# Performance work log

Measured on AMD Instinct MI355X. Metric: run time of the kernel, lower is better.

## Reference

```python
import jax, jax.numpy as jnp
import numpy as np

B, N, F_IN, F_OUT, H = 8, 1024, 256, 256, 4
HD = F_OUT // H  # head_dim = 64
NEG_SLOPE = 0.2


def setup_inputs() -> dict:
    key = jax.random.key(0)
    k1, k2, k3 = jax.random.split(key, 3)
    x = jax.random.normal(k1, (B, N, F_IN), dtype=jnp.float32)
    adj = jnp.ones((B, N, N), dtype=jnp.int32)
    # Linear weight, stored as [in, out] so h = x @ W
    W = jax.random.normal(k2, (F_IN, F_OUT), dtype=jnp.float32) / np.sqrt(F_IN)
    # attention vector a: [H, 2*head_dim], xavier-ish init
    a = jax.random.normal(k3, (H, 2 * HD), dtype=jnp.float32) * np.sqrt(2.0 / (H + 2 * HD))
    return {"x": x, "adj": adj, "W": W, "a": a}


def reference(x, adj, W, a):
    Bq, Nq, _ = x.shape
    h = (x @ W).reshape(Bq, Nq, H, HD).transpose(0, 2, 1, 3)  # [B,H,N,HD]
    a1, a2 = a[:, :HD], a[:, HD:]  # decompose concat: e_nm = h_n.a1 + h_m.a2
    s1 = jnp.einsum('bhnd,hd->bhn', h, a1)
    s2 = jnp.einsum('bhmd,hd->bhm', h, a2)
    e = jax.nn.leaky_relu(s1[:, :, :, None] + s2[:, :, None, :], NEG_SLOPE)  # [B,H,N,N]
    e = jnp.where(adj[:, None, :, :] == 0, -jnp.inf, e)
    attention = jax.nn.softmax(e, axis=-1)
    out = jnp.einsum('bhnm,bhmd->bhnd', attention, h)
    return out.transpose(0, 2, 1, 3).reshape(Bq, Nq, H * HD)
```

## Files before the change

### kernel.cpp

```cpp
#include <hip/hip_runtime.h>
#include <math.h>

#define H 4
#define HD 64
#define NN 1024
#define BB 8
#define FIN 256
#define FOUT 256

typedef _Float16 f16x8 __attribute__((ext_vector_type(8)));
typedef _Float16 f16x4 __attribute__((ext_vector_type(4)));
typedef _Float16 f16x2 __attribute__((ext_vector_type(2)));
typedef float f32x4 __attribute__((ext_vector_type(4)));

__global__ __launch_bounds__(256) void prep(const int* __restrict__ adj,
                                            unsigned* __restrict__ adjP,
                                            const float* __restrict__ W,
                                            _Float16* __restrict__ WT) {
  __shared__ float tile[64][68];
  const int tid = threadIdx.x;
  if (blockIdx.x < 1024) {
    size_t widx = (size_t)blockIdx.x * 256 + tid;
    const int4* p = (const int4*)adj + widx * 8;
    int4 v[8];
#pragma unroll
    for (int i = 0; i < 8; ++i) v[i] = p[i];
    unsigned bits = 0;
#pragma unroll
    for (int i = 0; i < 8; ++i) {
      bits |= (v[i].x != 0 ? 1u : 0u) << (4 * i);
      bits |= (v[i].y != 0 ? 2u : 0u) << (4 * i);
      bits |= (v[i].z != 0 ? 4u : 0u) << (4 * i);
      bits |= (v[i].w != 0 ? 8u : 0u) << (4 * i);
    }
    adjP[widx] = bits;
  } else {
    const int bx = blockIdx.x - 1024;
    const int k0 = (bx & 3) * 64, f0 = (bx >> 2) * 64;
    const int r = tid >> 4, c4 = (tid & 15) * 4;
#pragma unroll
    for (int p = 0; p < 4; ++p) {
      float4 v = *(const float4*)&W[(size_t)(k0 + p * 16 + r) * FOUT + f0 + c4];
      *(float4*)&tile[p * 16 + r][c4] = v;
    }
    __syncthreads();
    const int f = tid >> 2, kg = (tid & 3) * 16;
#pragma unroll
    for (int i = 0; i < 4; ++i) {
      f16x4 o;
#pragma unroll
      for (int j = 0; j < 4; ++j) o[j] = (_Float16)tile[kg + i * 4 + j][f];
      *(f16x4*)&WT[(size_t)(f0 + f) * FIN + k0 + kg + i * 4] = o;
    }
  }
}

__global__ __launch_bounds__(256) void gemm_xw(const float* __restrict__ x,
                                               const _Float16* __restrict__ WT,
                                               const float* __restrict__ a,
                                               _Float16* __restrict__ hT,
                                               float* __restrict__ s1_ws,
                                               float* __restrict__ s2_ws,
                                               float* __restrict__ u_ws,
                                               float* __restrict__ v_ws) {
  __shared__ _Float16 xs[64][264];
  const int tid = threadIdx.x;
  const int lane = tid & 63, w = tid >> 6;
  const int c = lane & 15, q = lane >> 4;
  const int bn0 = blockIdx.x * 64;
  const int head = blockIdx.y;
  const int b = bn0 >> 10, nb = bn0 & 1023;
  const int bh = b * H + head;

  float4 v[16];
#pragma unroll
  for (int p = 0; p < 16; ++p) {
    int f = p * 256 + tid;
    int row = f >> 6, col = (f & 63) * 4;
    v[p] = *(const float4*)&x[(size_t)(bn0 + row) * FIN + col];
  }
#pragma unroll
  for (int p = 0; p < 16; ++p) {
    int f = p * 256 + tid;
    int row = f >> 6, col = (f & 63) * 4;
    f16x4 h4;
    h4[0] = (_Float16)v[p].x; h4[1] = (_Float16)v[p].y;
    h4[2] = (_Float16)v[p].z; h4[3] = (_Float16)v[p].w;
    *(f16x4*)&xs[row][col] = h4;
  }
  __syncthreads();

  f32x4 acc[4];
#pragma unroll
  for (int t = 0; t < 4; ++t) acc[t] = (f32x4){0.f, 0.f, 0.f, 0.f};
  const _Float16* wbase = WT + (size_t)head * 64 * FIN;
#pragma unroll
  for (int ks = 0; ks < 8; ++ks) {
    f16x8 af = *(const f16x8*)&xs[w * 16 + c][ks * 32 + q * 8];
#pragma unroll
    for (int t = 0; t < 4; ++t) {
      f16x8 bf = *(const f16x8*)&wbase[(size_t)(t * 16 + c) * FIN + ks * 32 + q * 8];
      acc[t] = __builtin_amdgcn_mfma_f32_16x16x32_f16(af, bf, acc[t], 0, 0, 0);
    }
  }

  float a1v[4], a2v[4];
#pragma unroll
  for (int t = 0; t < 4; ++t) {
    a1v[t] = a[head * 2 * HD + t * 16 + c];
    a2v[t] = a[head * 2 * HD + HD + t * 16 + c];
  }
  float s1p[4] = {0.f, 0.f, 0.f, 0.f};
  float s2p[4] = {0.f, 0.f, 0.f, 0.f};
#pragma unroll
  for (int t = 0; t < 4; ++t) {
    f16x4 hv;
#pragma unroll
    for (int rr = 0; rr < 4; ++rr) {
      hv[rr] = (_Float16)acc[t][rr];
      s1p[rr] += acc[t][rr] * a1v[t];
      s2p[rr] += acc[t][rr] * a2v[t];
    }
    *(f16x4*)&hT[((size_t)(bh * 64 + t * 16 + c)) * NN + nb + w * 16 + q * 4] = hv;
  }
#pragma unroll
  for (int rr = 0; rr < 4; ++rr) {
    float s1 = s1p[rr], s2 = s2p[rr];
#pragma unroll
    for (int off = 8; off; off >>= 1) {
      s1 += __shfl_xor(s1, off);
      s2 += __shfl_xor(s2, off);
    }
    if (c == 0) {
      int n = nb + w * 16 + q * 4 + rr;
      size_t idx = (size_t)bh * NN + n;
      s1_ws[idx] = s1;
      s2_ws[idx] = s2;
      u_ws[idx] = __expf(s2);
      v_ws[idx] = __expf(0.2f * s2);
    }
  }
}

__global__ __launch_bounds__(256) void attn(const _Float16* __restrict__ hT,
                                            const float* __restrict__ s1_ws,
                                            const float* __restrict__ s2_ws,
                                            const float* __restrict__ u_ws,
                                            const float* __restrict__ v_ws,
                                            const unsigned* __restrict__ adjP,
                                            float* __restrict__ out) {
  __shared__ float s2r[NN], uu[NN], vv[NN];
  __shared__ unsigned adjT[32][32];
  __shared__ float accbuf[2][2][4][64][4];
  __shared__ float Mbuf[4];
  __shared__ float Lbuf[4][32];
  __shared__ float invLb[32];
  const int tid = threadIdx.x, lane = tid & 63, w = tid >> 6;
  const int c = lane & 15, q = lane >> 4;
  const int ntile = blockIdx.x, bh = blockIdx.y;
  const int b = bh >> 2, head = bh & 3;
  const int n0 = ntile * 32;
  const int K0 = w * 256, W0 = w * 8;

  float4 s2f;
  {
    size_t base = (size_t)bh * NN + tid * 4;
    s2f = *(const float4*)&s2_ws[base];
    *(float4*)&s2r[tid * 4] = s2f;
    *(float4*)&uu[tid * 4] = *(const float4*)&u_ws[base];
    *(float4*)&vv[tid * 4] = *(const float4*)&v_ws[base];
    const int row = tid >> 3, wd0 = (tid & 7) * 4;
    uint4 aw = *(const uint4*)&adjP[((size_t)(b * NN + n0 + row)) * 32 + wd0];
    adjT[wd0 + 0][row] = aw.x;
    adjT[wd0 + 1][row] = aw.y;
    adjT[wd0 + 2][row] = aw.z;
    adjT[wd0 + 3][row] = aw.w;
  }
  float tmax = fmaxf(fmaxf(s2f.x, s2f.y), fmaxf(s2f.z, s2f.w));
#pragma unroll
  for (int off = 32; off; off >>= 1) tmax = fmaxf(tmax, __shfl_xor(tmax, off));
  if (lane == 0) Mbuf[w] = tmax;
  float s1A = s1_ws[(size_t)bh * NN + n0 + c];
  float s1B = s1_ws[(size_t)bh * NN + n0 + 16 + c];
  __syncthreads();

  float mxall = fmaxf(fmaxf(Mbuf[0], Mbuf[1]), fmaxf(Mbuf[2], Mbuf[3]));
  float tA = s1A + mxall, tB = s1B + mxall;
  float MA = fmaxf(tA, 0.2f * tA);
  float MB = fmaxf(tB, 0.2f * tB);
  float ArowA = __expf(s1A - MA), BrowA = __expf(0.2f * s1A - MA), ns1A = -s1A;
  float ArowB = __expf(s1B - MB), BrowB = __expf(0.2f * s1B - MB), ns1B = -s1B;

  float LpA = 0.f, LpB = 0.f;
  f32x4 acc[2][4];
#pragma unroll
  for (int t = 0; t < 2; ++t)
#pragma unroll
    for (int d = 0; d < 4; ++d) acc[t][d] = (f32x4){0.f, 0.f, 0.f, 0.f};
  const _Float16* hbase = hT + (size_t)bh * 64 * NN + (size_t)c * NN + K0 + q * 8;

#pragma unroll 2
  for (int ks = 0; ks < 8; ++ks) {
    f16x8 bf0 = *(const f16x8*)(hbase + (size_t)0 * 16 * NN + ks * 32);
    f16x8 bf1 = *(const f16x8*)(hbase + (size_t)1 * 16 * NN + ks * 32);
    f16x8 bf2 = *(const f16x8*)(hbase + (size_t)2 * 16 * NN + ks * 32);
    f16x8 bf3 = *(const f16x8*)(hbase + (size_t)3 * 16 * NN + ks * 32);

    int m0 = K0 + ks * 32 + q * 8;
    f32x4 sa = *(const f32x4*)&s2r[m0];
    f32x4 sb = *(const f32x4*)&s2r[m0 + 4];
    f32x4 ua = *(const f32x4*)&uu[m0];
    f32x4 ub = *(const f32x4*)&uu[m0 + 4];
    f32x4 va = *(const f32x4*)&vv[m0];
    f32x4 vb = *(const f32x4*)&vv[m0 + 4];
    unsigned wdA = adjT[W0 + ks][c] >> (q * 8);
    unsigned wdB = adjT[W0 + ks][c + 16] >> (q * 8);

    float pA[8], pB[8];
#pragma unroll
    for (int j = 0; j < 4; ++j) {
      float a0 = (sa[j] >= ns1A) ? ArowA * ua[j] : BrowA * va[j];
      float a1 = (sb[j] >= ns1A) ? ArowA * ub[j] : BrowA * vb[j];
      pA[j] = ((wdA >> j) & 1u) ? a0 : 0.f;
      pA[j + 4] = ((wdA >> (j + 4)) & 1u) ? a1 : 0.f;
      float b0 = (sa[j] >= ns1B) ? ArowB * ua[j] : BrowB * va[j];
      float b1 = (sb[j] >= ns1B) ? ArowB * ub[j] : BrowB * vb[j];
      pB[j] = ((wdB >> j) & 1u) ? b0 : 0.f;
      pB[j + 4] = ((wdB >> (j + 4)) & 1u) ? b1 : 0.f;
    }
    LpA += ((pA[0] + pA[1]) + (pA[2] + pA[3])) + ((pA[4] + pA[5]) + (pA[6] + pA[7]));
    LpB += ((pB[0] + pB[1]) + (pB[2] + pB[3])) + ((pB[4] + pB[5]) + (pB[6] + pB[7]));

    union { f16x8 v8; f16x2 h2[4]; } PA, PB;
#pragma unroll
    for (int j = 0; j < 4; ++j) {
      PA.h2[j] = __builtin_bit_cast(f16x2, __builtin_amdgcn_cvt_pkrtz(pA[2 * j], pA[2 * j + 1]));
      PB.h2[j] = __builtin_bit_cast(f16x2, __builtin_amdgcn_cvt_pkrtz(pB[2 * j], pB[2 * j + 1]));
    }

    acc[0][0] = __builtin_amdgcn_mfma_f32_16x16x32_f16(PA.v8, bf0, acc[0][0], 0, 0, 0);
    acc[0][1] = __builtin_amdgcn_mfma_f32_16x16x32_f16(PA.v8, bf1, acc[0][1], 0, 0, 0);
    acc[0][2] = __builtin_amdgcn_mfma_f32_16x16x32_f16(PA.v8, bf2, acc[0][2], 0, 0, 0);
    acc[0][3] = __builtin_amdgcn_mfma_f32_16x16x32_f16(PA.v8, bf3, acc[0][3], 0, 0, 0);
    acc[1][0] = __builtin_amdgcn_mfma_f32_16x16x32_f16(PB.v8, bf0, acc[1][0], 0, 0, 0);
    acc[1][1] = __builtin_amdgcn_mfma_f32_16x16x32_f16(PB.v8, bf1, acc[1][1], 0, 0, 0);
    acc[1][2] = __builtin_amdgcn_mfma_f32_16x16x32_f16(PB.v8, bf2, acc[1][2], 0, 0, 0);
    acc[1][3] = __builtin_amdgcn_mfma_f32_16x16x32_f16(PB.v8, bf3, acc[1][3], 0, 0, 0);
  }

  LpA += __shfl_xor(LpA, 16);
  LpA += __shfl_xor(LpA, 32);
  LpB += __shfl_xor(LpB, 16);
  LpB += __shfl_xor(LpB, 32);
  if (lane < 16) {
    Lbuf[w][c] = LpA;
    Lbuf[w][16 + c] = LpB;
  }
  if (w >= 2) {
#pragma unroll
    for (int t = 0; t < 2; ++t)
#pragma unroll
      for (int d = 0; d < 4; ++d)
        *(f32x4*)&accbuf[w - 2][t][d][lane][0] = acc[t][d];
  }
  __syncthreads();
  if (w < 2) {
#pragma unroll
    for (int t = 0; t < 2; ++t)
#pragma unroll
      for (int d = 0; d < 4; ++d)
        acc[t][d] += *(const f32x4*)&accbuf[w][t][d][lane][0];
  }
  if (tid < 32) {
    float Ls = Lbuf[0][tid] + Lbuf[1][tid] + Lbuf[2][tid] + Lbuf[3][tid];
    invLb[tid] = 1.0f / Ls;
  }
  __syncthreads();
  if (w == 1) {
#pragma unroll
    for (int t = 0; t < 2; ++t)
#pragma unroll
      for (int d = 0; d < 4; ++d)
        *(f32x4*)&accbuf[0][t][d][lane][0] = acc[t][d];
  }
  __syncthreads();
  if (w == 0) {
#pragma unroll
    for (int t = 0; t < 2; ++t) {
#pragma unroll
      for (int d = 0; d < 4; ++d)
        acc[t][d] += *(const f32x4*)&accbuf[0][t][d][lane][0];
#pragma unroll
      for (int rr = 0; rr < 4; ++rr) {
        int nloc = t * 16 + q * 4 + rr;
        float il = invLb[nloc];
        size_t o = ((size_t)(b * NN + n0 + nloc)) * FOUT + head * 64;
#pragma unroll
        for (int d = 0; d < 4; ++d) out[o + d * 16 + c] = acc[t][d][rr] * il;
      }
    }
  }
}

extern "C" void kernel_launch(void* const* d_in, const int* in_sizes, int n_in,
                              void* d_out, int out_size, void* d_ws, size_t ws_size,
                              hipStream_t stream) {
  const float* x = (const float*)d_in[0];
  const int* adj = (const int*)d_in[1];
  const float* W = (const float*)d_in[2];
  const float* a = (const float*)d_in[3];
  float* out = (float*)d_out;

  char* ws = (char*)d_ws;
  _Float16* hT = (_Float16*)ws;
  _Float16* WT = (_Float16*)(ws + (size_t)4 * 1024 * 1024);
  float* s1_ws = (float*)(ws + (size_t)4 * 1024 * 1024 + 128 * 1024);
  float* s2_ws = s1_ws + (size_t)BB * H * NN;
  float* u_ws = s2_ws + (size_t)BB * H * NN;
  float* v_ws = u_ws + (size_t)BB * H * NN;
  unsigned* adjP = (unsigned*)(v_ws + (size_t)BB * H * NN);

  prep<<<1040, 256, 0, stream>>>(adj, adjP, W, WT);
  gemm_xw<<<dim3(128, 4), 256, 0, stream>>>(x, WT, a, hT, s1_ws, s2_ws, u_ws, v_ws);
  attn<<<dim3(32, 32), 256, 0, stream>>>(hT, s1_ws, s2_ws, u_ws, v_ws, adjP, out);
}
```

Measured before the change: 114.5 us.

## Fuse adjacency packing into the GEMM launch and load x fragments directly

The adjacency bit-packing work moves out of the prep kernel and becomes extra blocks of the x@W GEMM kernel, so the large adj read overlaps with the GEMM. The prep kernel now only transposes and converts W. The GEMM also drops its shared-memory staging of x: each lane loads its own fp32 fragment from global memory and converts it to fp16 in registers, which removes the LDS traffic and the barrier. The trade-off is less coalesced, partly redundant global loads of x across the four head blocks, and GEMM blocks now compete with packing blocks for compute units.

```diff
diff --git a/kernel.cpp b/kernel.cpp
--- a/kernel.cpp
+++ b/kernel.cpp
@@ -13,18 +13,48 @@
 typedef _Float16 f16x2 __attribute__((ext_vector_type(2)));
 typedef float f32x4 __attribute__((ext_vector_type(4)));
 
-__global__ __launch_bounds__(256) void prep(const int* __restrict__ adj,
-                                            unsigned* __restrict__ adjP,
-                                            const float* __restrict__ W,
-                                            _Float16* __restrict__ WT) {
+__global__ __launch_bounds__(256) void prep_w(const float* __restrict__ W,
+                                              _Float16* __restrict__ WT) {
   __shared__ float tile[64][68];
   const int tid = threadIdx.x;
-  if (blockIdx.x < 1024) {
-    size_t widx = (size_t)blockIdx.x * 256 + tid;
-    const int4* p = (const int4*)adj + widx * 8;
+  const int bx = blockIdx.x;
+  const int k0 = (bx & 3) * 64, f0 = (bx >> 2) * 64;
+  const int r = tid >> 4, c4 = (tid & 15) * 4;
+#pragma unroll
+  for (int p = 0; p < 4; ++p) {
+    float4 v = *(const float4*)&W[(size_t)(k0 + p * 16 + r) * FOUT + f0 + c4];
+    *(float4*)&tile[p * 16 + r][c4] = v;
+  }
+  __syncthreads();
+  const int f = tid >> 2, kg = (tid & 3) * 16;
+#pragma unroll
+  for (int i = 0; i < 4; ++i) {
+    f16x4 o;
+#pragma unroll
+    for (int j = 0; j < 4; ++j) o[j] = (_Float16)tile[kg + i * 4 + j][f];
+    *(f16x4*)&WT[(size_t)(f0 + f) * FIN + k0 + kg + i * 4] = o;
+  }
+}
+
+__global__ __launch_bounds__(256) void gemm_pack(const float* __restrict__ x,
+                                                 const _Float16* __restrict__ WT,
+                                                 const float* __restrict__ a,
+                                                 const int* __restrict__ adj,
+                                                 unsigned* __restrict__ adjP,
+                                                 _Float16* __restrict__ hT,
+                                                 float* __restrict__ s1_ws,
+                                                 float* __restrict__ s2_ws,
+                                                 float* __restrict__ u_ws,
+                                                 float* __restrict__ v_ws) {
+  const int tid = threadIdx.x;
+
+  if (blockIdx.x >= 128) {
+    const int p = (blockIdx.x - 128) + 256 * blockIdx.y;
+    size_t widx = (size_t)p * 256 + tid;
+    const int4* ap = (const int4*)adj + widx * 8;
     int4 v[8];
 #pragma unroll
-    for (int i = 0; i < 8; ++i) v[i] = p[i];
+    for (int i = 0; i < 8; ++i) v[i] = ap[i];
     unsigned bits = 0;
 #pragma unroll
     for (int i = 0; i < 8; ++i) {
@@ -34,37 +64,9 @@
       bits |= (v[i].w != 0 ? 8u : 0u) << (4 * i);
     }
     adjP[widx] = bits;
-  } else {
-    const int bx = blockIdx.x - 1024;
-    const int k0 = (bx & 3) * 64, f0 = (bx >> 2) * 64;
-    const int r = tid >> 4, c4 = (tid & 15) * 4;
-#pragma unroll
-    for (int p = 0; p < 4; ++p) {
-      float4 v = *(const float4*)&W[(size_t)(k0 + p * 16 + r) * FOUT + f0 + c4];
-      *(float4*)&tile[p * 16 + r][c4] = v;
-    }
-    __syncthreads();
-    const int f = tid >> 2, kg = (tid & 3) * 16;
-#pragma unroll
-    for (int i = 0; i < 4; ++i) {
-      f16x4 o;
-#pragma unroll
-      for (int j = 0; j < 4; ++j) o[j] = (_Float16)tile[kg + i * 4 + j][f];
-      *(f16x4*)&WT[(size_t)(f0 + f) * FIN + k0 + kg + i * 4] = o;
-    }
-  }
-}
-
-__global__ __launch_bounds__(256) void gemm_xw(const float* __restrict__ x,
-                                               const _Float16* __restrict__ WT,
-                                               const float* __restrict__ a,
-                                               _Float16* __restrict__ hT,
-                                               float* __restrict__ s1_ws,
-                                               float* __restrict__ s2_ws,
-                                               float* __restrict__ u_ws,
-                                               float* __restrict__ v_ws) {
-  __shared__ _Float16 xs[64][264];
-  const int tid = threadIdx.x;
+    return;
+  }
+
   const int lane = tid & 63, w = tid >> 6;
   const int c = lane & 15, q = lane >> 4;
   const int bn0 = blockIdx.x * 64;
@@ -72,31 +74,28 @@
   const int b = bn0 >> 10, nb = bn0 & 1023;
   const int bh = b * H + head;
 
-  float4 v[16];
-#pragma unroll
-  for (int p = 0; p < 16; ++p) {
-    int f = p * 256 + tid;
-    int row = f >> 6, col = (f & 63) * 4;
-    v[p] = *(const float4*)&x[(size_t)(bn0 + row) * FIN + col];
-  }
-#pragma unroll
-  for (int p = 0; p < 16; ++p) {
-    int f = p * 256 + tid;
-    int row = f >> 6, col = (f & 63) * 4;
-    f16x4 h4;
-    h4[0] = (_Float16)v[p].x; h4[1] = (_Float16)v[p].y;
-    h4[2] = (_Float16)v[p].z; h4[3] = (_Float16)v[p].w;
-    *(f16x4*)&xs[row][col] = h4;
-  }
-  __syncthreads();
+  const _Float16* wbase = WT + (size_t)head * 64 * FIN;
+  const float* xrow = x + (size_t)(bn0 + w * 16 + c) * FIN;
+
+  float4 xa[16];
+#pragma unroll
+  for (int ks = 0; ks < 8; ++ks) {
+    xa[2 * ks] = *(const float4*)&xrow[ks * 32 + q * 8];
+    xa[2 * ks + 1] = *(const float4*)&xrow[ks * 32 + q * 8 + 4];
+  }
 
   f32x4 acc[4];
 #pragma unroll
   for (int t = 0; t < 4; ++t) acc[t] = (f32x4){0.f, 0.f, 0.f, 0.f};
-  const _Float16* wbase = WT + (size_t)head * 64 * FIN;
+
 #pragma unroll
   for (int ks = 0; ks < 8; ++ks) {
-    f16x8 af = *(const f16x8*)&xs[w * 16 + c][ks * 32 + q * 8];
+    float4 u0 = xa[2 * ks], u1 = xa[2 * ks + 1];
+    f16x8 af;
+    af[0] = (_Float16)u0.x; af[1] = (_Float16)u0.y;
+    af[2] = (_Float16)u0.z; af[3] = (_Float16)u0.w;
+    af[4] = (_Float16)u1.x; af[5] = (_Float16)u1.y;
+    af[6] = (_Float16)u1.z; af[7] = (_Float16)u1.w;
 #pragma unroll
     for (int t = 0; t < 4; ++t) {
       f16x8 bf = *(const f16x8*)&wbase[(size_t)(t * 16 + c) * FIN + ks * 32 + q * 8];
@@ -320,7 +319,8 @@
   float* v_ws = u_ws + (size_t)BB * H * NN;
   unsigned* adjP = (unsigned*)(v_ws + (size_t)BB * H * NN);
 
-  prep<<<1040, 256, 0, stream>>>(adj, adjP, W, WT);
-  gemm_xw<<<dim3(128, 4), 256, 0, stream>>>(x, WT, a, hT, s1_ws, s2_ws, u_ws, v_ws);
+  prep_w<<<16, 256, 0, stream>>>(W, WT);
+  gemm_pack<<<dim3(384, 4), 256, 0, stream>>>(x, WT, a, adj, adjP, hT, s1_ws, s2_ws,
+                                              u_ws, v_ws);
   attn<<<dim3(32, 32), 256, 0, stream>>>(hT, s1_ws, s2_ws, u_ws, v_ws, adjP, out);
 }
```

Result: slower. 117.8 us (+2.9%).
